# Kernel optimization log

Measured on AMD Instinct MI355X. Metric: run time of the kernel, lower is better.

Reference implementation:

```python
import jax, jax.numpy as jnp
import numpy as np

B, S, D = 4, 1024, 1280
H, DH = 20, 64          # n_head, d_hidden = embed_dim // n_head
DF = 4 * D              # r_ff = 4


def setup_inputs() -> dict:
    key = jax.random.key(0)
    ks = jax.random.split(key, 8)
    s_qkv = 1.0 / np.sqrt(D)
    inp = {
        "x": jax.random.normal(ks[0], (B, S, D), dtype=jnp.float32),
        # projection weights stored [in, out] so y = x @ W
        "Wq": jax.random.normal(ks[1], (D, H * DH), dtype=jnp.float32) * s_qkv,
        "Wk": jax.random.normal(ks[2], (D, H * DH), dtype=jnp.float32) * s_qkv,
        "Wv": jax.random.normal(ks[3], (D, H * DH), dtype=jnp.float32) * s_qkv,
        "ln_g": jnp.ones((D,), dtype=jnp.float32),
        "ln_b": jnp.zeros((D,), dtype=jnp.float32),
        "W1": jax.random.normal(ks[4], (D, DF), dtype=jnp.float32) * np.sqrt(2.0 / D),
        "b1": jnp.zeros((DF,), dtype=jnp.float32),
        "W2": jax.random.normal(ks[5], (DF, D), dtype=jnp.float32) * (1.0 / np.sqrt(DF)),
        "b2": jnp.zeros((D,), dtype=jnp.float32),
    }
    return inp


def reference(x, Wq, Wk, Wv, ln_g, ln_b, W1, b1, W2, b2):
    scaling = 1.0 / np.sqrt(DH)
    # --- Attention (note: original forward never applies to_out) ---
    q = (x @ Wq).reshape(B, S, H, DH) * scaling
    k = (x @ Wk).reshape(B, S, H, DH)
    v = (x @ Wv).reshape(B, S, H, DH)
    attn = jnp.einsum('bqhd,bkhd->bhqk', q, k)
    attn = jax.nn.softmax(attn, axis=-1)
    out = jnp.einsum('bhqk,bkhd->bqhd', attn, v).reshape(B, S, H * DH)
    x = out + x  # residual
    # --- FeedForward: LayerNorm -> linear1 -> relu -> linear2, residual ---
    mu = jnp.mean(x, axis=-1, keepdims=True)
    var = jnp.mean(jnp.square(x - mu), axis=-1, keepdims=True)
    h = (x - mu) * jax.lax.rsqrt(var + 1e-5) * ln_g + ln_b
    h = jax.nn.relu(h @ W1 + b1)
    h = h @ W2 + b2
    return x + h
```

## Files before the change

### kernel.cpp

```cpp
#include <hip/hip_runtime.h>
#include <hip/hip_bf16.h>

typedef short bf16x8 __attribute__((ext_vector_type(8)));
typedef float f32x4 __attribute__((ext_vector_type(4)));

typedef unsigned int u32_as1 __attribute__((address_space(1)));
typedef unsigned int u32_as3 __attribute__((address_space(3)));

#define B_ 4
#define S_ 1024
#define D_ 1280
#define H_ 20
#define DH_ 64
#define DF_ 5120
#define BS_ (B_*S_)
#define NQKV 3840

__device__ __forceinline__ void gld_lds16(const __hip_bfloat16* g, __hip_bfloat16* l) {
  __builtin_amdgcn_global_load_lds((const u32_as1*)g, (u32_as3*)l, 16, 0, 0);
}

__global__ __launch_bounds__(256) void cvt_f2b(
    const float* __restrict__ in, __hip_bfloat16* __restrict__ out, int n4)
{
  int i = blockIdx.x * 256 + threadIdx.x;
  if (i >= n4) return;
  const float4 v = ((const float4*)in)[i];
  __hip_bfloat16 o[4] = {__float2bfloat16(v.x), __float2bfloat16(v.y),
                         __float2bfloat16(v.z), __float2bfloat16(v.w)};
  *(short4*)(out + (size_t)i * 4) = *(short4*)o;
}

__global__ __launch_bounds__(256) void transpose_f2b(
    const float* __restrict__ in, __hip_bfloat16* __restrict__ out,
    int K, int N)
{
  __shared__ float tile[32][33];
  int k0 = blockIdx.x * 32, n0 = blockIdx.y * 32;
  int tx = threadIdx.x & 31, ty = threadIdx.x >> 5;
  #pragma unroll
  for (int i = 0; i < 32; i += 8)
    tile[ty + i][tx] = in[(size_t)(k0 + ty + i) * N + n0 + tx];
  __syncthreads();
  #pragma unroll
  for (int i = 0; i < 32; i += 8)
    out[(size_t)(n0 + ty + i) * K + k0 + tx] = __float2bfloat16(tile[tx][ty + i]);
}

__global__ __launch_bounds__(256) void transpose_v(
    const __hip_bfloat16* __restrict__ qkv, __hip_bfloat16* __restrict__ vT)
{
  __shared__ __hip_bfloat16 tile[32][33];
  int s0 = blockIdx.x * 32;
  int d0 = blockIdx.y * 32;
  int bh = blockIdx.z;
  int b = bh / H_, h = bh - b * H_;
  int tx = threadIdx.x & 31, ty = threadIdx.x >> 5;
  const __hip_bfloat16* src = qkv + (size_t)b * S_ * NQKV + 2 * D_ + h * DH_;
  #pragma unroll
  for (int i = 0; i < 32; i += 8)
    tile[ty + i][tx] = src[(size_t)(s0 + ty + i) * NQKV + d0 + tx];
  __syncthreads();
  __hip_bfloat16* dst = vT + (size_t)bh * DH_ * S_;
  #pragma unroll
  for (int i = 0; i < 32; i += 8)
    dst[(size_t)(d0 + ty + i) * S_ + s0 + tx] = tile[tx][ty + i];
}

template<int EPI>
__global__ __launch_bounds__(256) void gemm_lds(
    const __hip_bfloat16* __restrict__ A,
    const __hip_bfloat16* __restrict__ BT,
    const float* __restrict__ bias,
    __hip_bfloat16* __restrict__ C,
    float* __restrict__ Cf0,
    float* __restrict__ Cf1,
    int M, int N, int K, int Kext)
{
  __shared__ __hip_bfloat16 As[128 * 32];
  __shared__ __hip_bfloat16 Bs[128 * 32];

  const int t = threadIdx.x;
  const int lane = t & 63;
  const int wave = t >> 6;
  const int wm = wave >> 1, wn = wave & 1;
  const int bm = blockIdx.x * 128, bn = blockIdx.y * 128;
  const int quad = lane >> 4, l16 = lane & 15;
  const int koff = blockIdx.z * Kext;

  const int srow = t >> 2;
  const int gc = (t & 3) ^ ((srow >> 1) & 3);
  const __hip_bfloat16* Ag = A  + (size_t)(bm + srow) * K + koff + gc * 8;
  const __hip_bfloat16* Bg = BT + (size_t)(bn + srow) * K + koff + gc * 8;
  const size_t rstep = (size_t)64 * K;
  __hip_bfloat16* Asl = As + t * 8;
  __hip_bfloat16* Bsl = Bs + t * 8;

  const int rsw = (l16 >> 1) & 3;
  const int rc = (quad ^ rsw) * 8;

  f32x4 acc[4][4];
  #pragma unroll
  for (int i = 0; i < 4; i++)
    #pragma unroll
    for (int j = 0; j < 4; j++)
      acc[i][j] = (f32x4){0.f, 0.f, 0.f, 0.f};

  for (int k0 = 0; k0 < Kext; k0 += 32) {
    gld_lds16(Ag + k0,         Asl);
    gld_lds16(Ag + rstep + k0, Asl + 2048);
    gld_lds16(Bg + k0,         Bsl);
    gld_lds16(Bg + rstep + k0, Bsl + 2048);
    __syncthreads();

    bf16x8 a[4], b[4];
    #pragma unroll
    for (int i = 0; i < 4; i++)
      a[i] = *(const bf16x8*)(As + (wm * 64 + i * 16 + l16) * 32 + rc);
    #pragma unroll
    for (int j = 0; j < 4; j++)
      b[j] = *(const bf16x8*)(Bs + (wn * 64 + j * 16 + l16) * 32 + rc);
    #pragma unroll
    for (int i = 0; i < 4; i++)
      #pragma unroll
      for (int j = 0; j < 4; j++)
        acc[i][j] = __builtin_amdgcn_mfma_f32_16x16x32_bf16(a[i], b[j], acc[i][j], 0, 0, 0);
    __syncthreads();
  }

  float* Cf = (blockIdx.z == 0) ? Cf0 : Cf1;
  #pragma unroll
  for (int i = 0; i < 4; i++) {
    #pragma unroll
    for (int j = 0; j < 4; j++) {
      int col = bn + wn * 64 + j * 16 + l16;
      #pragma unroll
      for (int r = 0; r < 4; r++) {
        int row = bm + wm * 64 + i * 16 + quad * 4 + r;
        float v = acc[i][j][r];
        if (EPI == 1) { v += bias[col]; v = fmaxf(v, 0.f); }
        if (EPI == 3) {
          Cf[(size_t)row * N + col] = v;
        } else {
          C[(size_t)row * N + col] = __float2bfloat16(v);
        }
      }
    }
  }
}

__global__ __launch_bounds__(256) void ffn2_reduce(
    const float* __restrict__ P0, const float* __restrict__ P1,
    const float* __restrict__ bias, const float* __restrict__ resid,
    float* __restrict__ out)
{
  int i = blockIdx.x * 256 + threadIdx.x;
  float4 p0 = ((const float4*)P0)[i];
  float4 p1 = ((const float4*)P1)[i];
  float4 r  = ((const float4*)resid)[i];
  float4 b  = ((const float4*)bias)[i % (D_ / 4)];
  float4 o;
  o.x = p0.x + p1.x + r.x + b.x;
  o.y = p0.y + p1.y + r.y + b.y;
  o.z = p0.z + p1.z + r.z + b.z;
  o.w = p0.w + p1.w + r.w + b.w;
  ((float4*)out)[i] = o;
}

__global__ __launch_bounds__(256) void attn_mfma(
    const __hip_bfloat16* __restrict__ qkv,
    const __hip_bfloat16* __restrict__ vT,
    const float* __restrict__ x,
    float* __restrict__ x1)
{
  const int qt = blockIdx.x, h = blockIdx.y, b = blockIdx.z;
  const int t = threadIdx.x;
  const int lane = t & 63;
  const int wave = t >> 6;
  const int quad = lane >> 4, l16 = lane & 15;

  __shared__ __hip_bfloat16 Ks[2][64 * 64];
  __shared__ __hip_bfloat16 Vs[2][64 * 64];
  __shared__ short Pl[4][16][72];

  const int qrow0 = qt * 128 + wave * 32;
  const size_t tok0 = (size_t)b * S_;
  const int qcol = h * DH_;
  const int kcol = D_ + h * DH_;
  const size_t vtbase = (size_t)(b * H_ + h) * DH_ * S_;

  const int s1i = t + 256;
  const int r0 = t >> 3,   c0 = (t & 7)   ^ (r0 & 7);
  const int r1 = s1i >> 3, c1 = (s1i & 7) ^ (r1 & 7);
  const __hip_bfloat16* Kg0 = qkv + (tok0 + r0) * NQKV + kcol + c0 * 8;
  const __hip_bfloat16* Kg1 = qkv + (tok0 + r1) * NQKV + kcol + c1 * 8;
  const __hip_bfloat16* Vg0 = vT + vtbase + (size_t)r0 * S_ + c0 * 8;
  const __hip_bfloat16* Vg1 = vT + vtbase + (size_t)r1 * S_ + c1 * 8;
  const size_t kstep = (size_t)64 * NQKV;

  const float qscale = 0.125f * 1.44269504088896340736f;
  bf16x8 aq[2][2];
  #pragma unroll
  for (int m = 0; m < 2; m++)
    #pragma unroll
    for (int kc = 0; kc < 2; kc++) {
      bf16x8 raw = *(const bf16x8*)(qkv + (tok0 + qrow0 + m * 16 + l16) * NQKV
                                        + qcol + kc * 32 + quad * 8);
      bf16x8 scaled;
      #pragma unroll
      for (int j = 0; j < 8; j++) {
        float f = __uint_as_float(((unsigned)(unsigned short)raw[j]) << 16) * qscale;
        __hip_bfloat16 hb = __float2bfloat16(f);
        scaled[j] = *reinterpret_cast<short*>(&hb);
      }
      aq[m][kc] = scaled;
    }

  f32x4 O[2][4];
  float lsum[2][4];
  #pragma unroll
  for (int m = 0; m < 2; m++)
    #pragma unroll
    for (int n = 0; n < 4; n++) O[m][n] = (f32x4){0.f, 0.f, 0.f, 0.f};
  #pragma unroll
  for (int m = 0; m < 2; m++)
    #pragma unroll
    for (int r = 0; r < 4; r++) lsum[m][r] = 0.f;

  gld_lds16(Kg0, &Ks[0][t * 8]);
  gld_lds16(Kg1, &Ks[0][t * 8 + 2048]);
  gld_lds16(Vg0, &Vs[0][t * 8]);
  gld_lds16(Vg1, &Vs[0][t * 8 + 2048]);

  const int fsw = l16 & 7;

  for (int kt = 0; kt < S_ / 64; kt++) {
    const int buf = kt & 1;
    __syncthreads();

    if (kt + 1 < S_ / 64) {
      const int nb = buf ^ 1;
      gld_lds16(Kg0 + (size_t)(kt + 1) * kstep, &Ks[nb][t * 8]);
      gld_lds16(Kg1 + (size_t)(kt + 1) * kstep, &Ks[nb][t * 8 + 2048]);
      gld_lds16(Vg0 + (kt + 1) * 64, &Vs[nb][t * 8]);
      gld_lds16(Vg1 + (kt + 1) * 64, &Vs[nb][t * 8 + 2048]);
    }

    bf16x8 kb[4][2];
    #pragma unroll
    for (int j = 0; j < 4; j++)
      #pragma unroll
      for (int kc = 0; kc < 2; kc++)
        kb[j][kc] = *(const bf16x8*)&Ks[buf][(j * 16 + l16) * 64
                                            + (((kc * 4 + quad) ^ fsw) * 8)];
    f32x4 sc[2][4];
    #pragma unroll
    for (int m = 0; m < 2; m++)
      #pragma unroll
      for (int j = 0; j < 4; j++) {
        sc[m][j] = (f32x4){0.f, 0.f, 0.f, 0.f};
        sc[m][j] = __builtin_amdgcn_mfma_f32_16x16x32_bf16(aq[m][0], kb[j][0], sc[m][j], 0, 0, 0);
        sc[m][j] = __builtin_amdgcn_mfma_f32_16x16x32_bf16(aq[m][1], kb[j][1], sc[m][j], 0, 0, 0);
      }

    bf16x8 vb[4][2];
    #pragma unroll
    for (int n = 0; n < 4; n++)
      #pragma unroll
      for (int kc = 0; kc < 2; kc++)
        vb[n][kc] = *(const bf16x8*)&Vs[buf][(n * 16 + l16) * 64
                                            + (((kc * 4 + quad) ^ fsw) * 8)];

    #pragma unroll
    for (int m = 0; m < 2; m++) {
      #pragma unroll
      for (int j = 0; j < 4; j++)
        #pragma unroll
        for (int r = 0; r < 4; r++) {
          float p = exp2f(sc[m][j][r]);
          lsum[m][r] += p;
          Pl[wave][quad * 4 + r][j * 16 + l16] = (short)(__float_as_uint(p) >> 16);
        }
      bf16x8 pa0 = *(const bf16x8*)&Pl[wave][l16][quad * 8];
      bf16x8 pa1 = *(const bf16x8*)&Pl[wave][l16][32 + quad * 8];
      #pragma unroll
      for (int n = 0; n < 4; n++) {
        O[m][n] = __builtin_amdgcn_mfma_f32_16x16x32_bf16(pa0, vb[n][0], O[m][n], 0, 0, 0);
        O[m][n] = __builtin_amdgcn_mfma_f32_16x16x32_bf16(pa1, vb[n][1], O[m][n], 0, 0, 0);
      }
    }
  }

  #pragma unroll
  for (int m = 0; m < 2; m++)
    #pragma unroll
    for (int r = 0; r < 4; r++) {
      float s = lsum[m][r];
      s += __shfl_xor(s, 1);
      s += __shfl_xor(s, 2);
      s += __shfl_xor(s, 4);
      s += __shfl_xor(s, 8);
      lsum[m][r] = 1.f / s;
    }

  #pragma unroll
  for (int m = 0; m < 2; m++)
    #pragma unroll
    for (int n = 0; n < 4; n++)
      #pragma unroll
      for (int r = 0; r < 4; r++) {
        size_t row = tok0 + qrow0 + m * 16 + quad * 4 + r;
        int col = qcol + n * 16 + l16;
        size_t idx = row * D_ + col;
        x1[idx] = O[m][n][r] * lsum[m][r] + x[idx];
      }
}

__global__ __launch_bounds__(256) void ln_kernel(
    const float* __restrict__ x1, const float* __restrict__ g,
    const float* __restrict__ bta, __hip_bfloat16* __restrict__ h)
{
  int row = blockIdx.x, t = threadIdx.x;
  __shared__ float red[256];
  float v[5];
  size_t base = (size_t)row * D_;
  #pragma unroll
  for (int i = 0; i < 5; i++) v[i] = x1[base + t + 256 * i];
  float s = v[0] + v[1] + v[2] + v[3] + v[4];
  red[t] = s; __syncthreads();
  for (int off = 128; off; off >>= 1) {
    if (t < off) red[t] += red[t + off];
    __syncthreads();
  }
  float mu = red[0] * (1.f / D_);
  __syncthreads();
  float sq = 0.f;
  #pragma unroll
  for (int i = 0; i < 5; i++) { float d = v[i] - mu; sq += d * d; }
  red[t] = sq; __syncthreads();
  for (int off = 128; off; off >>= 1) {
    if (t < off) red[t] += red[t + off];
    __syncthreads();
  }
  float rs = rsqrtf(red[0] * (1.f / D_) + 1e-5f);
  #pragma unroll
  for (int i = 0; i < 5; i++) {
    int c = t + 256 * i;
    float hv = (v[i] - mu) * rs * g[c] + bta[c];
    h[base + c] = __float2bfloat16(hv);
  }
}

extern "C" void kernel_launch(void* const* d_in, const int* in_sizes, int n_in,
                              void* d_out, int out_size, void* d_ws, size_t ws_size,
                              hipStream_t stream) {
  (void)in_sizes; (void)n_in; (void)out_size; (void)ws_size;
  const float* x   = (const float*)d_in[0];
  const float* Wq  = (const float*)d_in[1];
  const float* Wk  = (const float*)d_in[2];
  const float* Wv  = (const float*)d_in[3];
  const float* lng = (const float*)d_in[4];
  const float* lnb = (const float*)d_in[5];
  const float* W1  = (const float*)d_in[6];
  const float* b1  = (const float*)d_in[7];
  const float* W2  = (const float*)d_in[8];
  const float* b2  = (const float*)d_in[9];
  float* out = (float*)d_out;

  char* ws = (char*)d_ws;
  size_t o = 0;
  __hip_bfloat16* W2T = (__hip_bfloat16*)(ws + o); o += (size_t)D_ * DF_ * 2;
  float*          x1  = (float*)(ws + o);          o += (size_t)BS_ * D_ * 4;
  char* regA = ws + o; o += (size_t)DF_ * D_ * 2 + (size_t)BS_ * D_ * 2;
  __hip_bfloat16* W1T  = (__hip_bfloat16*)regA;
  __hip_bfloat16* hbuf = (__hip_bfloat16*)(regA + (size_t)DF_ * D_ * 2);
  float*          P0   = (float*)regA;
  char* regB = ws + o;
  __hip_bfloat16* xb    = (__hip_bfloat16*)regB;
  __hip_bfloat16* BTqkv = (__hip_bfloat16*)(regB + (size_t)BS_ * D_ * 2);
  __hip_bfloat16* qkv   = (__hip_bfloat16*)(regB + (size_t)BS_ * D_ * 2
                                                 + (size_t)NQKV * D_ * 2);
  __hip_bfloat16* vT    = (__hip_bfloat16*)(regB + (size_t)BS_ * D_ * 2
                                                 + (size_t)NQKV * D_ * 2
                                                 + (size_t)BS_ * NQKV * 2);
  float*          P1    = (float*)regB;
  __hip_bfloat16* gbuf  = (__hip_bfloat16*)(regB + (size_t)BS_ * D_ * 4);

  transpose_f2b<<<dim3(D_/32, D_/32), 256, 0, stream>>>(Wq, BTqkv,                   D_, D_);
  transpose_f2b<<<dim3(D_/32, D_/32), 256, 0, stream>>>(Wk, BTqkv + (size_t)D_*D_,   D_, D_);
  transpose_f2b<<<dim3(D_/32, D_/32), 256, 0, stream>>>(Wv, BTqkv + (size_t)2*D_*D_, D_, D_);
  transpose_f2b<<<dim3(D_/32, DF_/32), 256, 0, stream>>>(W1, W1T, D_, DF_);
  transpose_f2b<<<dim3(DF_/32, D_/32), 256, 0, stream>>>(W2, W2T, DF_, D_);
  cvt_f2b<<<(BS_*D_/4 + 255)/256, 256, 0, stream>>>(x, xb, BS_*D_/4);

  gemm_lds<0><<<dim3(BS_/128, NQKV/128), 256, 0, stream>>>(
      xb, BTqkv, nullptr, qkv, nullptr, nullptr, BS_, NQKV, D_, D_);
  transpose_v<<<dim3(S_/32, DH_/32, B_*H_), 256, 0, stream>>>(qkv, vT);
  attn_mfma<<<dim3(S_/128, H_, B_), 256, 0, stream>>>(qkv, vT, x, x1);
  ln_kernel<<<BS_, 256, 0, stream>>>(x1, lng, lnb, hbuf);
  gemm_lds<1><<<dim3(BS_/128, DF_/128), 256, 0, stream>>>(
      hbuf, W1T, b1, gbuf, nullptr, nullptr, BS_, DF_, D_, D_);
  gemm_lds<3><<<dim3(BS_/128, D_/128, 2), 256, 0, stream>>>(
      gbuf, W2T, nullptr, nullptr, P0, P1, BS_, D_, DF_, DF_/2);
  ffn2_reduce<<<BS_*D_/4/256, 256, 0, stream>>>(P0, P1, b2, x1, out);
}
```

Baseline: 454.8 us.

## Replace 128x128 GEMM with double-buffered 256x256 tile, 8-wave MFMA kernel

The three projection GEMMs move from a single-buffered 128x128x32 tile kernel with 4 waves to a 256x256x64 tile kernel with 8 waves. The new kernel double-buffers LDS and prefetches the next K slice with global_load_lds while the current one is consumed. It also uses an XOR swizzle over 8 chunks and s_setprio around the MFMA bursts. The aim is more data reuse per LDS load and hiding global-load latency behind compute. The cost is 128KB of LDS per block, which allows only one block per CU, and fewer blocks than CUs for the QKV and FFN2 grids.

```diff
diff --git a/kernel.cpp b/kernel.cpp
--- a/kernel.cpp
+++ b/kernel.cpp
@@ -68,7 +68,7 @@
 }
 
 template<int EPI>
-__global__ __launch_bounds__(256) void gemm_lds(
+__global__ __launch_bounds__(512, 2) void gemm256(
     const __hip_bfloat16* __restrict__ A,
     const __hip_bfloat16* __restrict__ BT,
     const float* __restrict__ bias,
@@ -77,66 +77,108 @@
     float* __restrict__ Cf1,
     int M, int N, int K, int Kext)
 {
-  __shared__ __hip_bfloat16 As[128 * 32];
-  __shared__ __hip_bfloat16 Bs[128 * 32];
+  __shared__ __align__(16) __hip_bfloat16 As[2][256 * 64];
+  __shared__ __align__(16) __hip_bfloat16 Bs[2][256 * 64];
 
   const int t = threadIdx.x;
   const int lane = t & 63;
   const int wave = t >> 6;
-  const int wm = wave >> 1, wn = wave & 1;
-  const int bm = blockIdx.x * 128, bn = blockIdx.y * 128;
+  const int wm = wave >> 2, wn = wave & 3;
   const int quad = lane >> 4, l16 = lane & 15;
+  const int bm = blockIdx.x * 256, bn = blockIdx.y * 256;
   const int koff = blockIdx.z * Kext;
-
-  const int srow = t >> 2;
-  const int gc = (t & 3) ^ ((srow >> 1) & 3);
-  const __hip_bfloat16* Ag = A  + (size_t)(bm + srow) * K + koff + gc * 8;
-  const __hip_bfloat16* Bg = BT + (size_t)(bn + srow) * K + koff + gc * 8;
-  const size_t rstep = (size_t)64 * K;
-  __hip_bfloat16* Asl = As + t * 8;
-  __hip_bfloat16* Bsl = Bs + t * 8;
-
-  const int rsw = (l16 >> 1) & 3;
-  const int rc = (quad ^ rsw) * 8;
-
-  f32x4 acc[4][4];
-  #pragma unroll
-  for (int i = 0; i < 4; i++)
+  const int NT = Kext >> 6;
+
+  const int srow = t >> 3;
+  const int cs = (t & 7) ^ (srow & 7);
+  const __hip_bfloat16* Ag = A  + (size_t)(bm + srow) * K + koff + cs * 8;
+  const __hip_bfloat16* Bg = BT + (size_t)(bn + srow) * K + koff + cs * 8;
+  const size_t rq = (size_t)64 * K;
+
+  const int fsw = l16 & 7;
+  const int aoff = (wm * 128 + l16) * 64;
+  const int boff = (wn * 64 + l16) * 64;
+
+  f32x4 acc[8][4];
+  #pragma unroll
+  for (int i = 0; i < 8; i++)
     #pragma unroll
     for (int j = 0; j < 4; j++)
       acc[i][j] = (f32x4){0.f, 0.f, 0.f, 0.f};
 
-  for (int k0 = 0; k0 < Kext; k0 += 32) {
-    gld_lds16(Ag + k0,         Asl);
-    gld_lds16(Ag + rstep + k0, Asl + 2048);
-    gld_lds16(Bg + k0,         Bsl);
-    gld_lds16(Bg + rstep + k0, Bsl + 2048);
-    __syncthreads();
-
-    bf16x8 a[4], b[4];
-    #pragma unroll
-    for (int i = 0; i < 4; i++)
-      a[i] = *(const bf16x8*)(As + (wm * 64 + i * 16 + l16) * 32 + rc);
-    #pragma unroll
-    for (int j = 0; j < 4; j++)
-      b[j] = *(const bf16x8*)(Bs + (wn * 64 + j * 16 + l16) * 32 + rc);
-    #pragma unroll
-    for (int i = 0; i < 4; i++)
+  #pragma unroll
+  for (int q = 0; q < 4; q++) gld_lds16(Ag + q * rq, &As[0][q * 4096 + t * 8]);
+  #pragma unroll
+  for (int q = 0; q < 4; q++) gld_lds16(Bg + q * rq, &Bs[0][q * 4096 + t * 8]);
+
+  for (int u = 0; u < NT; ++u) {
+    const int b = u & 1;
+    if (u + 1 < NT) {
+      const size_t ko = (size_t)(u + 1) * 64;
+      #pragma unroll
+      for (int q = 0; q < 4; q++)
+        gld_lds16(Ag + q * rq + ko, &As[b ^ 1][q * 4096 + t * 8]);
+      #pragma unroll
+      for (int q = 0; q < 4; q++)
+        gld_lds16(Bg + q * rq + ko, &Bs[b ^ 1][q * 4096 + t * 8]);
+      asm volatile("s_waitcnt vmcnt(8)" ::: "memory");
+    } else {
+      asm volatile("s_waitcnt vmcnt(0)" ::: "memory");
+    }
+    __builtin_amdgcn_s_barrier();
+    asm volatile("" ::: "memory");
+
+    const __hip_bfloat16* Ab = As[b];
+    const __hip_bfloat16* Bb = Bs[b];
+
+    #pragma unroll
+    for (int kk = 0; kk < 2; kk++) {
+      const int kc = (((kk << 2) + quad) ^ fsw) << 3;
+
+      bf16x8 av[4], bv[4];
+      #pragma unroll
+      for (int i = 0; i < 4; i++)
+        av[i] = *(const bf16x8*)(Ab + aoff + i * 1024 + kc);
       #pragma unroll
       for (int j = 0; j < 4; j++)
-        acc[i][j] = __builtin_amdgcn_mfma_f32_16x16x32_bf16(a[i], b[j], acc[i][j], 0, 0, 0);
-    __syncthreads();
+        bv[j] = *(const bf16x8*)(Bb + boff + j * 1024 + kc);
+      __builtin_amdgcn_s_barrier();
+      asm volatile("s_waitcnt lgkmcnt(0)" ::: "memory");
+      __builtin_amdgcn_s_setprio(1);
+      #pragma unroll
+      for (int i = 0; i < 4; i++)
+        #pragma unroll
+        for (int j = 0; j < 4; j++)
+          acc[i][j] = __builtin_amdgcn_mfma_f32_16x16x32_bf16(av[i], bv[j], acc[i][j], 0, 0, 0);
+      __builtin_amdgcn_s_setprio(0);
+      __builtin_amdgcn_s_barrier();
+
+      bf16x8 aw[4];
+      #pragma unroll
+      for (int i = 0; i < 4; i++)
+        aw[i] = *(const bf16x8*)(Ab + aoff + (i + 4) * 1024 + kc);
+      __builtin_amdgcn_s_barrier();
+      asm volatile("s_waitcnt lgkmcnt(0)" ::: "memory");
+      __builtin_amdgcn_s_setprio(1);
+      #pragma unroll
+      for (int i = 0; i < 4; i++)
+        #pragma unroll
+        for (int j = 0; j < 4; j++)
+          acc[i + 4][j] = __builtin_amdgcn_mfma_f32_16x16x32_bf16(aw[i], bv[j], acc[i + 4][j], 0, 0, 0);
+      __builtin_amdgcn_s_setprio(0);
+      __builtin_amdgcn_s_barrier();
+    }
   }
 
   float* Cf = (blockIdx.z == 0) ? Cf0 : Cf1;
   #pragma unroll
-  for (int i = 0; i < 4; i++) {
+  for (int i = 0; i < 8; i++) {
     #pragma unroll
     for (int j = 0; j < 4; j++) {
       int col = bn + wn * 64 + j * 16 + l16;
       #pragma unroll
       for (int r = 0; r < 4; r++) {
-        int row = bm + wm * 64 + i * 16 + quad * 4 + r;
+        int row = bm + wm * 128 + i * 16 + quad * 4 + r;
         float v = acc[i][j][r];
         if (EPI == 1) { v += bias[col]; v = fmaxf(v, 0.f); }
         if (EPI == 3) {
@@ -393,14 +435,14 @@
   transpose_f2b<<<dim3(DF_/32, D_/32), 256, 0, stream>>>(W2, W2T, DF_, D_);
   cvt_f2b<<<(BS_*D_/4 + 255)/256, 256, 0, stream>>>(x, xb, BS_*D_/4);
 
-  gemm_lds<0><<<dim3(BS_/128, NQKV/128), 256, 0, stream>>>(
+  gemm256<0><<<dim3(BS_/256, NQKV/256), 512, 0, stream>>>(
       xb, BTqkv, nullptr, qkv, nullptr, nullptr, BS_, NQKV, D_, D_);
   transpose_v<<<dim3(S_/32, DH_/32, B_*H_), 256, 0, stream>>>(qkv, vT);
   attn_mfma<<<dim3(S_/128, H_, B_), 256, 0, stream>>>(qkv, vT, x, x1);
   ln_kernel<<<BS_, 256, 0, stream>>>(x1, lng, lnb, hbuf);
-  gemm_lds<1><<<dim3(BS_/128, DF_/128), 256, 0, stream>>>(
+  gemm256<1><<<dim3(BS_/256, DF_/256), 512, 0, stream>>>(
       hbuf, W1T, b1, gbuf, nullptr, nullptr, BS_, DF_, D_, D_);
-  gemm_lds<3><<<dim3(BS_/128, D_/128, 2), 256, 0, stream>>>(
+  gemm256<3><<<dim3(BS_/256, D_/256, 2), 512, 0, stream>>>(
       gbuf, W2T, nullptr, nullptr, P0, P1, BS_, D_, DF_, DF_/2);
   ffn2_reduce<<<BS_*D_/4/256, 256, 0, stream>>>(P0, P1, b2, x1, out);
 }
```

Result: slower. 478.0 us (+5.1%).

## Replace GEMM with 256x256 double-buffered pipelined kernel using 8 waves

Applied to the files above, without the earlier changes.

Swaps the simple 128x128 single-buffered GEMM for a 256x256 tile kernel with 512 threads, double-buffered LDS, and K-steps of 64 split into two halves. Global-to-LDS loads for later tiles are issued between MFMA phases, with explicit vmcnt waits, barriers and setprio, so memory latency overlaps compute and more data is reused per tile. The cost is 128KB of LDS and higher register pressure. The larger tiles also give far fewer blocks for the FFN2 and QKV GEMMs (e.g. 16x5x2=160 for FFN2), so some CUs may sit idle.

```diff
diff --git a/kernel.cpp b/kernel.cpp
--- a/kernel.cpp
+++ b/kernel.cpp
@@ -68,7 +68,7 @@
 }
 
 template<int EPI>
-__global__ __launch_bounds__(256) void gemm_lds(
+__global__ __launch_bounds__(512, 2) void gemm256(
     const __hip_bfloat16* __restrict__ A,
     const __hip_bfloat16* __restrict__ BT,
     const float* __restrict__ bias,
@@ -77,66 +77,122 @@
     float* __restrict__ Cf1,
     int M, int N, int K, int Kext)
 {
-  __shared__ __hip_bfloat16 As[128 * 32];
-  __shared__ __hip_bfloat16 Bs[128 * 32];
+  __shared__ __align__(16) __hip_bfloat16 As[2][2][256 * 32];
+  __shared__ __align__(16) __hip_bfloat16 Bs[2][2][256 * 32];
+  __hip_bfloat16* AsF = &As[0][0][0];
+  __hip_bfloat16* BsF = &Bs[0][0][0];
 
   const int t = threadIdx.x;
   const int lane = t & 63;
   const int wave = t >> 6;
-  const int wm = wave >> 1, wn = wave & 1;
-  const int bm = blockIdx.x * 128, bn = blockIdx.y * 128;
+  const int wm = wave >> 2, wn = wave & 3;
   const int quad = lane >> 4, l16 = lane & 15;
+  const int bm = blockIdx.x * 256, bn = blockIdx.y * 256;
   const int koff = blockIdx.z * Kext;
+  const int Kc = (K - koff < Kext) ? (K - koff) : Kext;
+  const int NT = Kc >> 6;
 
   const int srow = t >> 2;
-  const int gc = (t & 3) ^ ((srow >> 1) & 3);
-  const __hip_bfloat16* Ag = A  + (size_t)(bm + srow) * K + koff + gc * 8;
-  const __hip_bfloat16* Bg = BT + (size_t)(bn + srow) * K + koff + gc * 8;
-  const size_t rstep = (size_t)64 * K;
-  __hip_bfloat16* Asl = As + t * 8;
-  __hip_bfloat16* Bsl = Bs + t * 8;
-
-  const int rsw = (l16 >> 1) & 3;
-  const int rc = (quad ^ rsw) * 8;
-
-  f32x4 acc[4][4];
-  #pragma unroll
-  for (int i = 0; i < 4; i++)
+  const int sc = (t & 3) ^ ((t >> 3) & 3);
+  const __hip_bfloat16* Ag = A  + (size_t)(bm + srow) * K + koff + sc * 8;
+  const __hip_bfloat16* Bg = BT + (size_t)(bn + srow) * K + koff + sc * 8;
+  const size_t rq = (size_t)128 * K;
+
+  const int swz = quad ^ ((l16 >> 1) & 3);
+  const int aob = (wm * 128 + l16) * 32 + swz * 8;
+  const int bob = (wn * 64 + l16) * 32 + swz * 8;
+
+  f32x4 acc[8][4];
+  #pragma unroll
+  for (int i = 0; i < 8; i++)
     #pragma unroll
     for (int j = 0; j < 4; j++)
       acc[i][j] = (f32x4){0.f, 0.f, 0.f, 0.f};
 
-  for (int k0 = 0; k0 < Kext; k0 += 32) {
-    gld_lds16(Ag + k0,         Asl);
-    gld_lds16(Ag + rstep + k0, Asl + 2048);
-    gld_lds16(Bg + k0,         Bsl);
-    gld_lds16(Bg + rstep + k0, Bsl + 2048);
-    __syncthreads();
-
-    bf16x8 a[4], b[4];
-    #pragma unroll
-    for (int i = 0; i < 4; i++)
-      a[i] = *(const bf16x8*)(As + (wm * 64 + i * 16 + l16) * 32 + rc);
-    #pragma unroll
-    for (int j = 0; j < 4; j++)
-      b[j] = *(const bf16x8*)(Bs + (wn * 64 + j * 16 + l16) * 32 + rc);
-    #pragma unroll
-    for (int i = 0; i < 4; i++)
-      #pragma unroll
-      for (int j = 0; j < 4; j++)
-        acc[i][j] = __builtin_amdgcn_mfma_f32_16x16x32_bf16(a[i], b[j], acc[i][j], 0, 0, 0);
-    __syncthreads();
-  }
+#define STAGE_A(u_, kk_, b_) do { \
+    const __hip_bfloat16* g_ = Ag + (size_t)(u_) * 64 + (kk_) * 32; \
+    gld_lds16(g_,      AsF + ((b_) * 2 + (kk_)) * 8192 + t * 8); \
+    gld_lds16(g_ + rq, AsF + ((b_) * 2 + (kk_)) * 8192 + 4096 + t * 8); \
+  } while (0)
+#define STAGE_B(u_, kk_, b_) do { \
+    const __hip_bfloat16* g_ = Bg + (size_t)(u_) * 64 + (kk_) * 32; \
+    gld_lds16(g_,      BsF + ((b_) * 2 + (kk_)) * 8192 + t * 8); \
+    gld_lds16(g_ + rq, BsF + ((b_) * 2 + (kk_)) * 8192 + 4096 + t * 8); \
+  } while (0)
+
+  STAGE_A(0, 0, 0); STAGE_B(0, 0, 0); STAGE_A(0, 1, 0); STAGE_B(0, 1, 0);
+  STAGE_B(1, 0, 1); STAGE_A(1, 0, 1); STAGE_B(1, 1, 1);
+  asm volatile("s_waitcnt vmcnt(6)" ::: "memory");
+  __builtin_amdgcn_s_barrier();
+  asm volatile("" ::: "memory");
+
+  bf16x8 av[4], bv[4];
+
+#define PHASE_MFMA(ibase_) \
+    __builtin_amdgcn_s_barrier(); \
+    asm volatile("s_waitcnt lgkmcnt(0)" ::: "memory"); \
+    __builtin_amdgcn_s_setprio(1); \
+    _Pragma("unroll") \
+    for (int i = 0; i < 4; i++) \
+      _Pragma("unroll") \
+      for (int j = 0; j < 4; j++) \
+        acc[(ibase_) + i][j] = __builtin_amdgcn_mfma_f32_16x16x32_bf16(av[i], bv[j], acc[(ibase_) + i][j], 0, 0, 0); \
+    __builtin_amdgcn_s_setprio(0); \
+    __builtin_amdgcn_s_barrier(); \
+    asm volatile("" ::: "memory");
+
+#define TILE_BODY(u_, B_) do { \
+    const int hb0 = (B_) * 2 * 8192, hb1 = ((B_) * 2 + 1) * 8192; \
+     \
+    _Pragma("unroll") \
+    for (int i = 0; i < 4; i++) av[i] = *(const bf16x8*)(AsF + hb0 + aob + i * 512); \
+    _Pragma("unroll") \
+    for (int j = 0; j < 4; j++) bv[j] = *(const bf16x8*)(BsF + hb0 + bob + j * 512); \
+    if ((u_) + 1 < NT) STAGE_A((u_) + 1, 1, (B_) ^ 1); \
+    PHASE_MFMA(0) \
+     \
+    _Pragma("unroll") \
+    for (int i = 0; i < 4; i++) av[i] = *(const bf16x8*)(AsF + hb0 + aob + (i + 4) * 512); \
+    if ((u_) + 2 < NT) STAGE_B((u_) + 2, 0, (B_)); \
+    PHASE_MFMA(4) \
+     \
+    _Pragma("unroll") \
+    for (int i = 0; i < 4; i++) av[i] = *(const bf16x8*)(AsF + hb1 + aob + i * 512); \
+    _Pragma("unroll") \
+    for (int j = 0; j < 4; j++) bv[j] = *(const bf16x8*)(BsF + hb1 + bob + j * 512); \
+    if ((u_) + 2 < NT) STAGE_A((u_) + 2, 0, (B_)); \
+    PHASE_MFMA(0) \
+     \
+    _Pragma("unroll") \
+    for (int i = 0; i < 4; i++) av[i] = *(const bf16x8*)(AsF + hb1 + aob + (i + 4) * 512); \
+    if ((u_) + 2 < NT) { \
+      STAGE_B((u_) + 2, 1, (B_)); \
+      asm volatile("s_waitcnt vmcnt(6)" ::: "memory"); \
+    } else { \
+      asm volatile("s_waitcnt vmcnt(0)" ::: "memory"); \
+    } \
+    PHASE_MFMA(4) \
+  } while (0)
+
+  for (int u = 0; u < NT; u += 2) {
+    TILE_BODY(u, 0);
+    TILE_BODY(u + 1, 1);
+  }
+
+#undef TILE_BODY
+#undef PHASE_MFMA
+#undef STAGE_A
+#undef STAGE_B
 
   float* Cf = (blockIdx.z == 0) ? Cf0 : Cf1;
   #pragma unroll
-  for (int i = 0; i < 4; i++) {
+  for (int i = 0; i < 8; i++) {
     #pragma unroll
     for (int j = 0; j < 4; j++) {
       int col = bn + wn * 64 + j * 16 + l16;
       #pragma unroll
       for (int r = 0; r < 4; r++) {
-        int row = bm + wm * 64 + i * 16 + quad * 4 + r;
+        int row = bm + wm * 128 + i * 16 + quad * 4 + r;
         float v = acc[i][j][r];
         if (EPI == 1) { v += bias[col]; v = fmaxf(v, 0.f); }
         if (EPI == 3) {
@@ -393,14 +449,14 @@
   transpose_f2b<<<dim3(DF_/32, D_/32), 256, 0, stream>>>(W2, W2T, DF_, D_);
   cvt_f2b<<<(BS_*D_/4 + 255)/256, 256, 0, stream>>>(x, xb, BS_*D_/4);
 
-  gemm_lds<0><<<dim3(BS_/128, NQKV/128), 256, 0, stream>>>(
+  gemm256<0><<<dim3(BS_/256, NQKV/256), 512, 0, stream>>>(
       xb, BTqkv, nullptr, qkv, nullptr, nullptr, BS_, NQKV, D_, D_);
   transpose_v<<<dim3(S_/32, DH_/32, B_*H_), 256, 0, stream>>>(qkv, vT);
   attn_mfma<<<dim3(S_/128, H_, B_), 256, 0, stream>>>(qkv, vT, x, x1);
   ln_kernel<<<BS_, 256, 0, stream>>>(x1, lng, lnb, hbuf);
-  gemm_lds<1><<<dim3(BS_/128, DF_/128), 256, 0, stream>>>(
+  gemm256<1><<<dim3(BS_/256, DF_/256), 512, 0, stream>>>(
       hbuf, W1T, b1, gbuf, nullptr, nullptr, BS_, DF_, D_, D_);
-  gemm_lds<3><<<dim3(BS_/128, D_/128, 2), 256, 0, stream>>>(
+  gemm256<3><<<dim3(BS_/256, D_/256, 2), 512, 0, stream>>>(
       gbuf, W2T, nullptr, nullptr, P0, P1, BS_, D_, DF_, DF_/2);
   ffn2_reduce<<<BS_*D_/4/256, 256, 0, stream>>>(P0, P1, b2, x1, out);
 }
```

Result: faster. 426.7 us (-6.2%).

## Double-buffer GEMM LDS tiles and enlarge block to 256x128 with 8 waves

Applied to the files above, without the earlier changes.

Replaces the single-buffered 128x128 GEMM with a 256x128 tile computed by 512 threads (8 waves) and two LDS buffers. The next K-slice's global-to-LDS loads are issued before the current slice is consumed, using explicit vmcnt waits and raw barriers, and MFMA issue gets raised priority. The aim is to hide global load latency behind MFMA work and reuse each B tile across more rows. The cost is twice the LDS per block and fewer blocks on the small GEMMs, and the loop assumes an even number of K tiles.

```diff
diff --git a/kernel.cpp b/kernel.cpp
--- a/kernel.cpp
+++ b/kernel.cpp
@@ -68,7 +68,7 @@
 }
 
 template<int EPI>
-__global__ __launch_bounds__(256) void gemm_lds(
+__global__ __launch_bounds__(512, 4) void gemm_bk32(
     const __hip_bfloat16* __restrict__ A,
     const __hip_bfloat16* __restrict__ BT,
     const float* __restrict__ bias,
@@ -77,27 +77,27 @@
     float* __restrict__ Cf1,
     int M, int N, int K, int Kext)
 {
-  __shared__ __hip_bfloat16 As[128 * 32];
-  __shared__ __hip_bfloat16 Bs[128 * 32];
+  __shared__ __align__(16) __hip_bfloat16 As[2][256 * 32];
+  __shared__ __align__(16) __hip_bfloat16 Bs[2][128 * 32];
 
   const int t = threadIdx.x;
   const int lane = t & 63;
   const int wave = t >> 6;
   const int wm = wave >> 1, wn = wave & 1;
-  const int bm = blockIdx.x * 128, bn = blockIdx.y * 128;
   const int quad = lane >> 4, l16 = lane & 15;
+  const int bm = blockIdx.x * 256, bn = blockIdx.y * 128;
   const int koff = blockIdx.z * Kext;
+  const int NT = Kext >> 5;
 
   const int srow = t >> 2;
-  const int gc = (t & 3) ^ ((srow >> 1) & 3);
-  const __hip_bfloat16* Ag = A  + (size_t)(bm + srow) * K + koff + gc * 8;
-  const __hip_bfloat16* Bg = BT + (size_t)(bn + srow) * K + koff + gc * 8;
-  const size_t rstep = (size_t)64 * K;
-  __hip_bfloat16* Asl = As + t * 8;
-  __hip_bfloat16* Bsl = Bs + t * 8;
-
-  const int rsw = (l16 >> 1) & 3;
-  const int rc = (quad ^ rsw) * 8;
+  const int sc = (t & 3) ^ ((t >> 3) & 3);
+  const __hip_bfloat16* Ag = A  + (size_t)(bm + srow) * K + koff + sc * 8;
+  const __hip_bfloat16* Bg = BT + (size_t)(bn + srow) * K + koff + sc * 8;
+  const size_t rqa = (size_t)128 * K;
+
+  const int swz = quad ^ ((l16 >> 1) & 3);
+  const int aob = (wm * 64 + l16) * 32 + swz * 8;
+  const int bob = (wn * 64 + l16) * 32 + swz * 8;
 
   f32x4 acc[4][4];
   #pragma unroll
@@ -106,27 +106,50 @@
     for (int j = 0; j < 4; j++)
       acc[i][j] = (f32x4){0.f, 0.f, 0.f, 0.f};
 
-  for (int k0 = 0; k0 < Kext; k0 += 32) {
-    gld_lds16(Ag + k0,         Asl);
-    gld_lds16(Ag + rstep + k0, Asl + 2048);
-    gld_lds16(Bg + k0,         Bsl);
-    gld_lds16(Bg + rstep + k0, Bsl + 2048);
-    __syncthreads();
-
-    bf16x8 a[4], b[4];
-    #pragma unroll
-    for (int i = 0; i < 4; i++)
-      a[i] = *(const bf16x8*)(As + (wm * 64 + i * 16 + l16) * 32 + rc);
-    #pragma unroll
-    for (int j = 0; j < 4; j++)
-      b[j] = *(const bf16x8*)(Bs + (wn * 64 + j * 16 + l16) * 32 + rc);
-    #pragma unroll
-    for (int i = 0; i < 4; i++)
-      #pragma unroll
-      for (int j = 0; j < 4; j++)
-        acc[i][j] = __builtin_amdgcn_mfma_f32_16x16x32_bf16(a[i], b[j], acc[i][j], 0, 0, 0);
-    __syncthreads();
-  }
+#define STAGE(u_, b_) do { \
+    const __hip_bfloat16* ga_ = Ag + (size_t)(u_) * 32; \
+    gld_lds16(ga_,       &As[b_][t * 8]); \
+    gld_lds16(ga_ + rqa, &As[b_][4096 + t * 8]); \
+    gld_lds16(Bg + (size_t)(u_) * 32, &Bs[b_][t * 8]); \
+  } while (0)
+
+#define STEP(u_, b_, last_) do { \
+    if (last_) { asm volatile("s_waitcnt vmcnt(0)" ::: "memory"); } \
+    else       { asm volatile("s_waitcnt vmcnt(3)" ::: "memory"); } \
+    __builtin_amdgcn_s_barrier(); \
+    asm volatile("" ::: "memory"); \
+    bf16x8 av[4], bv[4]; \
+    _Pragma("unroll") \
+    for (int i = 0; i < 4; i++) av[i] = *(const bf16x8*)(&As[b_][0] + aob + i * 512); \
+    _Pragma("unroll") \
+    for (int j = 0; j < 4; j++) bv[j] = *(const bf16x8*)(&Bs[b_][0] + bob + j * 512); \
+    __builtin_amdgcn_s_setprio(1); \
+    _Pragma("unroll") \
+    for (int i = 0; i < 4; i++) \
+      _Pragma("unroll") \
+      for (int j = 0; j < 4; j++) \
+        acc[i][j] = __builtin_amdgcn_mfma_f32_16x16x32_bf16(av[i], bv[j], acc[i][j], 0, 0, 0); \
+    __builtin_amdgcn_s_setprio(0); \
+    asm volatile("" ::: "memory"); \
+    __builtin_amdgcn_s_barrier(); \
+    asm volatile("" ::: "memory"); \
+  } while (0)
+
+  STAGE(0, 0);
+
+  for (int u = 0; u < NT; u += 2) {
+    STAGE(u + 1, 1);
+    STEP(u, 0, false);
+    if (u + 2 < NT) {
+      STAGE(u + 2, 0);
+      STEP(u + 1, 1, false);
+    } else {
+      STEP(u + 1, 1, true);
+    }
+  }
+
+#undef STEP
+#undef STAGE
 
   float* Cf = (blockIdx.z == 0) ? Cf0 : Cf1;
   #pragma unroll
@@ -393,14 +416,14 @@
   transpose_f2b<<<dim3(DF_/32, D_/32), 256, 0, stream>>>(W2, W2T, DF_, D_);
   cvt_f2b<<<(BS_*D_/4 + 255)/256, 256, 0, stream>>>(x, xb, BS_*D_/4);
 
-  gemm_lds<0><<<dim3(BS_/128, NQKV/128), 256, 0, stream>>>(
+  gemm_bk32<0><<<dim3(BS_/256, NQKV/128), 512, 0, stream>>>(
       xb, BTqkv, nullptr, qkv, nullptr, nullptr, BS_, NQKV, D_, D_);
   transpose_v<<<dim3(S_/32, DH_/32, B_*H_), 256, 0, stream>>>(qkv, vT);
   attn_mfma<<<dim3(S_/128, H_, B_), 256, 0, stream>>>(qkv, vT, x, x1);
   ln_kernel<<<BS_, 256, 0, stream>>>(x1, lng, lnb, hbuf);
-  gemm_lds<1><<<dim3(BS_/128, DF_/128), 256, 0, stream>>>(
+  gemm_bk32<1><<<dim3(BS_/256, DF_/128), 512, 0, stream>>>(
       hbuf, W1T, b1, gbuf, nullptr, nullptr, BS_, DF_, D_, D_);
-  gemm_lds<3><<<dim3(BS_/128, D_/128, 2), 256, 0, stream>>>(
+  gemm_bk32<3><<<dim3(BS_/256, D_/128, 2), 512, 0, stream>>>(
       gbuf, W2T, nullptr, nullptr, P0, P1, BS_, D_, DF_, DF_/2);
   ffn2_reduce<<<BS_*D_/4/256, 256, 0, stream>>>(P0, P1, b2, x1, out);
 }
```

Result: slower. 1.380 ms (+203.4%).
